# Kernel tuning notes

Measured on AMD Instinct MI355X. Metric: run time of the kernel, lower is better.

## Reference

```python
import jax, jax.numpy as jnp
import numpy as np

N, H, W, PD, HID, NH = 2, 64, 64, 16, 128, 4
EPS = 1e-5


def _bn(x, g, b):
    # training-mode BatchNorm over (N, H, W) with biased variance, channels last
    m = jnp.mean(x, axis=(0, 1, 2), keepdims=True)
    v = jnp.var(x, axis=(0, 1, 2), keepdims=True)
    return (x - m) * jax.lax.rsqrt(v + EPS) * g + b


def _mha(x, in_w, in_b, out_w, out_b, nh):
    # torch nn.MultiheadAttention (batch_first) with packed qkv in_proj
    B, S, E = x.shape
    hd = E // nh
    q, k, v = jnp.split(x @ in_w.T + in_b, 3, axis=-1)
    def heads(t):
        return t.reshape(B, S, nh, hd).transpose(0, 2, 1, 3)  # B,nh,S,hd
    q, k, v = heads(q), heads(k), heads(v)
    a = jax.nn.softmax(jnp.einsum('bnqd,bnkd->bnqk', q, k) / np.float32(np.sqrt(hd)), axis=-1)
    o = jnp.einsum('bnqk,bnkd->bnqd', a, v).transpose(0, 2, 1, 3).reshape(B, S, E)
    return o @ out_w.T + out_b


def setup_inputs():
    key = jax.random.key(0)
    ks = jax.random.split(key, 32)
    def r(i, shape, s=0.1):
        return jax.random.normal(ks[i], shape, dtype=jnp.float32) * s
    mask = (jnp.arange(W) % 2) == 0  # alternating columns kept, M = W//2
    return {
        'kspace': jax.random.normal(ks[0], (N, 2, H, W), dtype=jnp.float32),
        'mask': mask,
        'pre_conv_w': r(1, (PD, 2), 0.5), 'pre_conv_b': r(2, (PD,)),
        'pre_pe_H': r(3, (H, PD)), 'pre_pe_W': r(4, (W, PD)),
        'res_conv1_w': r(5, (PD, PD), 0.2), 'res_conv1_b': r(6, (PD,)),
        'res_bn1_g': 1.0 + r(7, (PD,)), 'res_bn1_b': r(8, (PD,)),
        'res_conv2_w': r(9, (PD, PD), 0.2), 'res_conv2_b': r(10, (PD,)),
        'res_bn2_g': 1.0 + r(11, (PD,)), 'res_bn2_b': r(12, (PD,)),
        'proj_w': r(13, (HID, PD), 0.2), 'proj_b': r(14, (HID,)),
        'enc_in_w': r(15, (3 * HID, HID), 0.08), 'enc_in_b': r(16, (3 * HID,)),
        'enc_out_w': r(17, (HID, HID), 0.08), 'enc_out_b': r(18, (HID,)),
        'dec_pe_H': r(19, (H, HID)), 'dec_pe_W': r(20, (W, HID)),
        'dec_in_w': r(21, (3 * HID, HID), 0.08), 'dec_in_b': r(22, (3 * HID,)),
        'dec_out_w': r(23, (HID, HID), 0.08), 'dec_out_b': r(24, (HID,)),
        'masked_token': r(25, (HID,), 1.0),
        'post_w': r(26, (2, HID), 0.1), 'post_b': r(27, (2,)),
    }


def reference(kspace, mask, pre_conv_w, pre_conv_b, pre_pe_H, pre_pe_W,
              res_conv1_w, res_conv1_b, res_bn1_g, res_bn1_b,
              res_conv2_w, res_conv2_b, res_bn2_g, res_bn2_b,
              proj_w, proj_b, enc_in_w, enc_in_b, enc_out_w, enc_out_b,
              dec_pe_H, dec_pe_W, dec_in_w, dec_in_b, dec_out_w, dec_out_b,
              masked_token, post_w, post_b):
    cols = np.nonzero(np.asarray(mask))[0]  # static sampled columns
    M = cols.shape[0]
    # gather valid columns; channels last: [N, H, M, 2]
    x = kspace.transpose(0, 2, 3, 1)[:, :, cols, :]
    h = x @ pre_conv_w.T + pre_conv_b  # 1x1 conv -> [N, H, M, PD]
    h = h + (pre_pe_H[:, None, :] + pre_pe_W[cols][None, :, :])
    # PixelwiseConstantChannelResNet (1 layer)
    r1 = jax.nn.relu(_bn(h @ res_conv1_w.T + res_conv1_b, res_bn1_g, res_bn1_b))
    r2 = jax.nn.relu(_bn(r1 @ res_conv2_w.T + res_conv2_b, res_bn2_g, res_bn2_b))
    h = jax.nn.relu(h + r2)
    h = h @ proj_w.T + proj_b  # [N, H, M, HID]
    enc = _mha(h.reshape(N, H * M, HID), enc_in_w, enc_in_b, enc_out_w, enc_out_b, NH)
    # scatter: fill unmasked positions with masked_token, masked with encoder output
    dec = jnp.broadcast_to(masked_token, (N, H, W, HID))
    dec = dec.at[:, :, cols, :].set(enc.reshape(N, H, M, HID))
    dec = dec + (dec_pe_H[:, None, :] + dec_pe_W[None, :, :])
    dec = _mha(dec.reshape(N, H * W, HID), dec_in_w, dec_in_b, dec_out_w, dec_out_b, NH)
    out = dec.reshape(N, H, W, HID) @ post_w.T + post_b  # [N, H, W, 2]
    return out.transpose(0, 3, 1, 2)  # [N, 2, H, W]
```

## Files before the change

kernel.cpp:

```cpp
#include <hip/hip_runtime.h>
#include <math.h>

#define N_ 2
#define H_ 64
#define W_ 64
#define M_ 32
#define PD_ 16
#define HID_ 128
#define NH_ 4
#define HD_ 32
#define S_ENC 2048
#define S_DEC 4096
#define EPS_ 1e-5f
#define SCALE_ 0.17677669529663687f
#define SCALE2_ (0.17677669529663687f * 1.4426950408889634f)

#define OFF_H     0
#define OFF_T1    65536
#define OFF_T2    131072
#define OFF_STAT  196608
#define OFF_WP    196672
#define OFF_BP    202816
#define OFF_QBF   203264
#define OFF_KBF   727552
#define OFF_VTBF  1251840
#define OFF_ATTBF 1776128
#define OFF_XBF2  2300416
#define OFF_WBF   2824704

#define WOFF_ENC_OUT 0
#define WOFF_DEC_IN  16384
#define WOFF_DEC_OUT 65536

#define IB_MF   2048
#define IB_WC   320
#define IB_WP   24
#define IB_BP   2
#define IB_TOT  (IB_MF + IB_WC + IB_WP + IB_BP + 1)

typedef short bf16x8 __attribute__((ext_vector_type(8)));
typedef short bf16x4 __attribute__((ext_vector_type(4)));
typedef float f32x4 __attribute__((ext_vector_type(4)));

__device__ __forceinline__ short f2bf(float f) {
  union { float f; unsigned u; } v; v.f = f;
  unsigned r = v.u + 0x7FFFu + ((v.u >> 16) & 1u);
  return (short)(r >> 16);
}

__global__ void k_init(const float* __restrict__ eow, const float* __restrict__ dw,
                       const float* __restrict__ dow, const float* __restrict__ mt,
                       const float* __restrict__ peH, const float* __restrict__ peW,
                       const float* __restrict__ ew, const float* __restrict__ pw,
                       const float* __restrict__ pb, const float* __restrict__ eib,
                       short* __restrict__ wbf, short* __restrict__ xdec,
                       float* __restrict__ wp, float* __restrict__ bp,
                       float* __restrict__ stat) {
  int blk = blockIdx.x, tid = threadIdx.x;
  if (blk < IB_MF) {
    int idx = blk * 256 + tid;
    int j = idx & 127;
    int widx = (idx >> 7) & 31;
    int hh = (idx >> 12) & 63;
    int b = idx >> 18;
    int w = 2 * widx + 1;
    xdec[((size_t)(b * 4096 + hh * 64 + w)) * 128 + j] =
        f2bf(mt[j] + peH[hh * 128 + j] + peW[w * 128 + j]);
  } else if (blk < IB_MF + IB_WC) {
    int idx = (blk - IB_MF) * 256 + tid;
    float v;
    if (idx < 16384) v = eow[idx];
    else if (idx < 65536) v = dw[idx - 16384];
    else v = dow[idx - 65536];
    wbf[idx] = f2bf(v);
  } else if (blk < IB_MF + IB_WC + IB_WP) {
    int e = (blk - IB_MF - IB_WC) * 256 + tid;
    int row = e >> 4, k = e & 15;
    float a = 0.f;
    for (int j = 0; j < 128; j++) a = fmaf(ew[row * 128 + j], pw[j * 16 + k], a);
    wp[e] = a;
  } else if (blk < IB_MF + IB_WC + IB_WP + IB_BP) {
    int row = (blk - IB_MF - IB_WC - IB_WP) * 256 + tid;
    if (row < 384) {
      float a = eib[row];
      for (int j = 0; j < 128; j++) a = fmaf(ew[row * 128 + j], pb[j], a);
      bp[row] = a;
    }
  } else {
    if (tid < 64) stat[tid] = 0.f;
  }
}

__global__ void k_prelin_stats(const float* __restrict__ ks, const float* __restrict__ pcw,
                               const float* __restrict__ pcb, const float* __restrict__ peH,
                               const float* __restrict__ peW, const float* __restrict__ w1,
                               const float* __restrict__ b1, float* __restrict__ h,
                               float* __restrict__ t1, float* __restrict__ stat) {
  int tid = threadIdx.x;
  int pos = blockIdx.x * 256 + tid;
  int m = pos & 31, hh = (pos >> 5) & 63, b = pos >> 11;
  int w = 2 * m;
  float x0 = ks[((b * 2 + 0) * H_ + hh) * W_ + w];
  float x1 = ks[((b * 2 + 1) * H_ + hh) * W_ + w];
  float hv[16], tv[16];
#pragma unroll
  for (int c = 0; c < 16; c++)
    hv[c] = x0 * pcw[c * 2] + x1 * pcw[c * 2 + 1] + pcb[c]
            + peH[hh * PD_ + c] + peW[w * PD_ + c];
#pragma unroll
  for (int c = 0; c < 16; c += 4)
    *(float4*)&h[pos * 16 + c] = make_float4(hv[c], hv[c + 1], hv[c + 2], hv[c + 3]);
#pragma unroll
  for (int c = 0; c < 16; c++) {
    float a = b1[c];
#pragma unroll
    for (int k = 0; k < 16; k++) a = fmaf(hv[k], w1[c * 16 + k], a);
    tv[c] = a;
    t1[pos * 16 + c] = a;
  }
  __shared__ float tl[256][17];
#pragma unroll
  for (int c = 0; c < 16; c++) tl[tid][c] = tv[c];
  __syncthreads();
  int c = tid & 15, g = tid >> 4;
  float s = 0.f, s2 = 0.f;
#pragma unroll
  for (int r = 0; r < 16; r++) {
    float v = tl[g * 16 + r][c];
    s += v; s2 += v * v;
  }
  __shared__ float ps[16][16], ps2[16][16];
  ps[g][c] = s; ps2[g][c] = s2;
  __syncthreads();
  if (tid < 16) {
    float S = 0.f, S2 = 0.f;
#pragma unroll
    for (int g2 = 0; g2 < 16; g2++) { S += ps[g2][tid]; S2 += ps2[g2][tid]; }
    atomicAdd(&stat[tid], S);
    atomicAdd(&stat[16 + tid], S2);
  }
}

__global__ void k_bnlin_stats(const float* __restrict__ t1, const float* __restrict__ stat,
                              const float* __restrict__ g1, const float* __restrict__ bb1,
                              const float* __restrict__ w2, const float* __restrict__ b2,
                              float* __restrict__ t2, float* __restrict__ statw) {
  int tid = threadIdx.x;
  int pos = blockIdx.x * 256 + tid;
  const float inv = 1.f / 4096.f;
  float r[16];
#pragma unroll
  for (int k = 0; k < 16; k++) {
    float mu = stat[k] * inv;
    float var = stat[16 + k] * inv - mu * mu;
    float v = (t1[pos * 16 + k] - mu) * rsqrtf(var + EPS_) * g1[k] + bb1[k];
    r[k] = fmaxf(v, 0.f);
  }
  float tv[16];
#pragma unroll
  for (int c = 0; c < 16; c++) {
    float a = b2[c];
#pragma unroll
    for (int k = 0; k < 16; k++) a = fmaf(r[k], w2[c * 16 + k], a);
    tv[c] = a;
    t2[pos * 16 + c] = a;
  }
  __shared__ float tl[256][17];
#pragma unroll
  for (int c = 0; c < 16; c++) tl[tid][c] = tv[c];
  __syncthreads();
  int c = tid & 15, g = tid >> 4;
  float s = 0.f, s2 = 0.f;
#pragma unroll
  for (int rr = 0; rr < 16; rr++) {
    float v = tl[g * 16 + rr][c];
    s += v; s2 += v * v;
  }
  __shared__ float ps[16][16], ps2[16][16];
  ps[g][c] = s; ps2[g][c] = s2;
  __syncthreads();
  if (tid < 16) {
    float S = 0.f, S2 = 0.f;
#pragma unroll
    for (int g2 = 0; g2 < 16; g2++) { S += ps[g2][tid]; S2 += ps2[g2][tid]; }
    atomicAdd(&statw[32 + tid], S);
    atomicAdd(&statw[48 + tid], S2);
  }
}

__global__ __launch_bounds__(256)
void k_fqkv_enc(const float* __restrict__ h, const float* __restrict__ t2,
                const float* __restrict__ stat, const float* __restrict__ g2,
                const float* __restrict__ bb2, const float* __restrict__ wp,
                const float* __restrict__ bp, short* __restrict__ qbf,
                short* __restrict__ kbf, short* __restrict__ vtbf) {
  int tid = threadIdx.x;
  int p0 = blockIdx.x * 32;
  __shared__ float hf[32][20];
  const float inv = 1.f / 4096.f;
#pragma unroll
  for (int i = 0; i < 2; i++) {
    int idx = tid * 2 + i;
    int lp = idx >> 4, c = idx & 15;
    int pos = p0 + lp;
    float mu = stat[32 + c] * inv;
    float var = stat[48 + c] * inv - mu * mu;
    float v = (t2[pos * 16 + c] - mu) * rsqrtf(var + EPS_) * g2[c] + bb2[c];
    v = fmaxf(v, 0.f);
    hf[lp][c] = fmaxf(h[pos * 16 + c] + v, 0.f);
  }
  __syncthreads();
  int bb = p0 >> 11;
  int sbase = p0 & 2047;
  {
    int col = tid;
    float wc[16];
#pragma unroll
    for (int k = 0; k < 16; k += 4) *(float4*)&wc[k] = *(const float4*)&wp[col * 16 + k];
    float bpv = bp[col];
    int isQ = (col < 128);
    int c2 = isQ ? col : (col - 128);
    int hd = c2 >> 5, d = c2 & 31;
    short* dst = isQ ? qbf : kbf;
    float sc = isQ ? SCALE2_ : 1.f;
    size_t rowb = ((size_t)(bb * 4 + hd) * S_ENC + sbase) * 32 + d;
    for (int lp = 0; lp < 32; lp++) {
      float a = bpv;
#pragma unroll
      for (int k = 0; k < 16; k++) a = fmaf(hf[lp][k], wc[k], a);
      dst[rowb + (size_t)lp * 32] = f2bf(a * sc);
    }
  }
  if (tid < 128) {
    int col = 256 + tid;
    float wc[16];
#pragma unroll
    for (int k = 0; k < 16; k += 4) *(float4*)&wc[k] = *(const float4*)&wp[col * 16 + k];
    float bpv = bp[col];
    int c2 = tid;
    int hd = c2 >> 5, d = c2 & 31;
    size_t rowb = ((size_t)(bb * 4 + hd) * 32 + d) * S_ENC + sbase;
    for (int lp4 = 0; lp4 < 32; lp4 += 4) {
      bf16x4 pk;
#pragma unroll
      for (int r = 0; r < 4; r++) {
        float a = bpv;
#pragma unroll
        for (int k = 0; k < 16; k++) a = fmaf(hf[lp4 + r][k], wc[k], a);
        pk[r] = f2bf(a);
      }
      *(bf16x4*)&vtbf[rowb + lp4] = pk;
    }
  }
}

#define MGEMM_STAGE_AND_FRAGS                                                   \
  __shared__ short As[64 * 128];                                                \
  __shared__ short Wl[64 * 128];                                                \
  int tid = threadIdx.x;                                                        \
  _Pragma("unroll")                                                             \
  for (int i = 0; i < 4; i++) {                                                 \
    int idx = i * 256 + tid;                                                    \
    int row = idx >> 4, c = idx & 15, slot = c ^ (row & 7);                     \
    *(bf16x8*)&As[row * 128 + slot * 8] =                                       \
        *(const bf16x8*)&abf[(size_t)(rb + row) * 128 + c * 8];                 \
    *(bf16x8*)&Wl[row * 128 + slot * 8] =                                       \
        *(const bf16x8*)&wbf[(size_t)(ob + row) * 128 + c * 8];                 \
  }                                                                             \
  __syncthreads();                                                              \
  int lane = tid & 63, wv = tid >> 6;                                           \
  int l15 = lane & 15, quad = lane >> 4;                                        \
  int m0 = wv * 16;                                                             \
  f32x4 acc[4];                                                                 \
  acc[0] = acc[1] = acc[2] = acc[3] = (f32x4){0.f, 0.f, 0.f, 0.f};              \
  _Pragma("unroll")                                                             \
  for (int kk = 0; kk < 4; kk++) {                                              \
    int sl = ((kk * 4 + quad) ^ (l15 & 7)) * 8;                                 \
    bf16x8 af = *(const bf16x8*)&As[(m0 + l15) * 128 + sl];                     \
    _Pragma("unroll")                                                           \
    for (int nt = 0; nt < 4; nt++) {                                            \
      bf16x8 wf = *(const bf16x8*)&Wl[(nt * 16 + l15) * 128 + sl];              \
      acc[nt] = __builtin_amdgcn_mfma_f32_16x16x32_bf16(af, wf, acc[nt], 0, 0, 0); \
    }                                                                           \
  }

__global__ __launch_bounds__(256)
void k_mgemm_qkv_dec(const short* __restrict__ abf, const short* __restrict__ wbf,
                     const float* __restrict__ bias, short* __restrict__ qbf,
                     short* __restrict__ kbf, short* __restrict__ vtbf) {
  const int S = 4096;
  int rb = blockIdx.x * 64, ob = blockIdx.y * 64;
  MGEMM_STAGE_AND_FRAGS
#pragma unroll
  for (int nt = 0; nt < 4; nt++) {
    int col = ob + nt * 16 + l15;
    float bv = bias[col];
    if (ob < 128) {
      int hd = col >> 5, d = col & 31;
#pragma unroll
      for (int r = 0; r < 4; r++) {
        int grow = rb + m0 + quad * 4 + r;
        int bb = grow >> 12, s = grow & (S - 1);
        qbf[((size_t)(bb * 4 + hd) * S + s) * 32 + d] =
            f2bf((acc[nt][r] + bv) * SCALE2_);
      }
    } else if (ob < 256) {
      int c2 = col - 128, hd = c2 >> 5, d = c2 & 31;
#pragma unroll
      for (int r = 0; r < 4; r++) {
        int grow = rb + m0 + quad * 4 + r;
        int bb = grow >> 12, s = grow & (S - 1);
        kbf[((size_t)(bb * 4 + hd) * S + s) * 32 + d] = f2bf(acc[nt][r] + bv);
      }
    } else {
      int c2 = col - 256, hd = c2 >> 5, d = c2 & 31;
      int grow0 = rb + m0 + quad * 4;
      int bb = grow0 >> 12, s0 = grow0 & (S - 1);
      bf16x4 pk;
#pragma unroll
      for (int r = 0; r < 4; r++) pk[r] = f2bf(acc[nt][r] + bv);
      *(bf16x4*)&vtbf[((size_t)(bb * 4 + hd) * 32 + d) * S + s0] = pk;
    }
  }
}

__global__ __launch_bounds__(256)
void k_mgemm_out_enc(const short* __restrict__ abf, const short* __restrict__ wbf,
                     const float* __restrict__ bias, const float* __restrict__ peH,
                     const float* __restrict__ peW, short* __restrict__ xdec) {
  int rb = blockIdx.x * 64, ob = blockIdx.y * 64;
  MGEMM_STAGE_AND_FRAGS
#pragma unroll
  for (int nt = 0; nt < 4; nt++) {
    int col = ob + nt * 16 + l15;
    float bv = bias[col];
#pragma unroll
    for (int r = 0; r < 4; r++) {
      int grow = rb + m0 + quad * 4 + r;
      int bb = grow >> 11, rem = grow & 2047;
      int hhh = rem >> 5, m = rem & 31, w = 2 * m;
      xdec[((size_t)(bb * 4096 + hhh * 64 + w)) * 128 + col] =
          f2bf(acc[nt][r] + bv + peH[hhh * 128 + col] + peW[w * 128 + col]);
    }
  }
}

__global__ __launch_bounds__(256)
void k_mgemm_out_post(const short* __restrict__ abf, const short* __restrict__ wbf,
                      const float* __restrict__ bias, const float* __restrict__ pw,
                      const float* __restrict__ pb, float* __restrict__ outp) {
  int rb = blockIdx.x * 64;
  __shared__ short As[64 * 128];
  __shared__ short Wl[128 * 128];
  int tid = threadIdx.x;
#pragma unroll
  for (int i = 0; i < 4; i++) {
    int idx = i * 256 + tid;
    int row = idx >> 4, c = idx & 15, slot = c ^ (row & 7);
    *(bf16x8*)&As[row * 128 + slot * 8] =
        *(const bf16x8*)&abf[(size_t)(rb + row) * 128 + c * 8];
  }
#pragma unroll
  for (int i = 0; i < 8; i++) {
    int idx = i * 256 + tid;
    int row = idx >> 4, c = idx & 15, slot = c ^ (row & 7);
    *(bf16x8*)&Wl[row * 128 + slot * 8] =
        *(const bf16x8*)&wbf[(size_t)row * 128 + c * 8];
  }
  __syncthreads();
  int lane = tid & 63, wv = tid >> 6;
  int l15 = lane & 15, quad = lane >> 4;
  int m0 = wv * 16;
  f32x4 acc[8];
#pragma unroll
  for (int nt = 0; nt < 8; nt++) acc[nt] = (f32x4){0.f, 0.f, 0.f, 0.f};
#pragma unroll
  for (int kk = 0; kk < 4; kk++) {
    int sl = ((kk * 4 + quad) ^ (l15 & 7)) * 8;
    bf16x8 af = *(const bf16x8*)&As[(m0 + l15) * 128 + sl];
#pragma unroll
    for (int nt = 0; nt < 8; nt++) {
      bf16x8 wf = *(const bf16x8*)&Wl[(nt * 16 + l15) * 128 + sl];
      acc[nt] = __builtin_amdgcn_mfma_f32_16x16x32_bf16(af, wf, acc[nt], 0, 0, 0);
    }
  }
  float bv[8], pw0[8], pw1[8];
#pragma unroll
  for (int nt = 0; nt < 8; nt++) {
    int col = nt * 16 + l15;
    bv[nt] = bias[col];
    pw0[nt] = pw[col];
    pw1[nt] = pw[128 + col];
  }
  float pb0 = pb[0], pb1 = pb[1];
#pragma unroll
  for (int r = 0; r < 4; r++) {
    float pc0 = 0.f, pc1 = 0.f;
#pragma unroll
    for (int nt = 0; nt < 8; nt++) {
      float yv = acc[nt][r] + bv[nt];
      pc0 = fmaf(yv, pw0[nt], pc0);
      pc1 = fmaf(yv, pw1[nt], pc1);
    }
    pc0 += __shfl_xor(pc0, 1); pc0 += __shfl_xor(pc0, 2);
    pc0 += __shfl_xor(pc0, 4); pc0 += __shfl_xor(pc0, 8);
    pc1 += __shfl_xor(pc1, 1); pc1 += __shfl_xor(pc1, 2);
    pc1 += __shfl_xor(pc1, 4); pc1 += __shfl_xor(pc1, 8);
    if (l15 == 0) {
      int grow = rb + m0 + quad * 4 + r;
      int bb = grow >> 12, hw = grow & 4095;
      outp[(size_t)(bb * 2 + 0) * 4096 + hw] = pc0 + pb0;
      outp[(size_t)(bb * 2 + 1) * 4096 + hw] = pc1 + pb1;
    }
  }
}

template <int S>
__global__ __launch_bounds__(1024)
__attribute__((amdgpu_waves_per_eu(8)))
void k_attn11(const short* __restrict__ qbf, const short* __restrict__ kbf,
              const short* __restrict__ vtbf, short* __restrict__ outb) {
  __shared__ __align__(16) char smem[65536];
  short* kb4 = (short*)smem;
  short* vt4 = (short*)(smem + 32768);
  float* abuf = (float*)smem;
  float* lb   = (float*)(smem + 24576);

  int qt = blockIdx.x, hh = blockIdx.y, b = blockIdx.z;
  int tid = threadIdx.x;
  int lane = tid & 63;
  int wv = tid >> 6;
  int qtr = wv >> 2;
  int wv4 = wv & 3;
  int l15 = lane & 15, quad = lane >> 4;
  int t256 = tid & 255;

  int bh = b * NH_ + hh;
  const short* kg = kbf + (size_t)bh * S * 32;
  const short* vg = vtbf + (size_t)bh * 32 * S;
  short* kbh = kb4 + qtr * 2048;
  short* vth = vt4 + qtr * 2048;

  bf16x8 qf = *(const bf16x8*)&qbf[((size_t)bh * S + qt * 64 + wv4 * 16 + l15) * 32
                                   + quad * 8];

  f32x4 acc[2];
  acc[0] = (f32x4){0.f, 0.f, 0.f, 0.f};
  acc[1] = (f32x4){0.f, 0.f, 0.f, 0.f};
  float lpart = 0.f;

  int srowK = t256 >> 2, schK = t256 & 3;
  int slotK = schK ^ ((srowK >> 1) & 3);
  int srowV = t256 >> 3, sslV = t256 & 7;
  int sgV = sslV ^ (srowV & 7);
  int gbV = ((sgV >> 2) << 5) + ((sgV & 3) << 2);

  int kq0 = qtr * (S / 4);
  int kxor = (l15 >> 1) & 3;
  int vsl = l15 & 7;

  const short* kgp = kg + (size_t)(kq0 + srowK) * 32 + schK * 8;
  const short* vgp0 = vg + (size_t)srowV * S + kq0 + gbV;
  const short* vgp1 = vgp0 + 16;
  short* kdst = kbh + srowK * 32 + slotK * 8;
  short* vdst = vth + srowV * 64 + sslV * 8;

  bf16x8 krg = *(const bf16x8*)kgp;
  bf16x4 vr0 = *(const bf16x4*)vgp0;
  bf16x4 vr1 = *(const bf16x4*)vgp1;

  constexpr int NIT = S / 256;
  for (int it = 0; it < NIT; ++it) {
    int co = (it & 1) << 13;
    *(bf16x8*)(kdst + co) = krg;
    *(bf16x8*)(vdst + co) = __builtin_shufflevector(vr0, vr1, 0, 1, 2, 3, 4, 5, 6, 7);
    if (it + 1 < NIT) {
      kgp += 64 * 32;
      vgp0 += 64;
      vgp1 += 64;
      krg = *(const bf16x8*)kgp;
      vr0 = *(const bf16x4*)vgp0;
      vr1 = *(const bf16x4*)vgp1;
    }
    asm volatile("s_waitcnt lgkmcnt(0)" ::: "memory");
    __builtin_amdgcn_s_barrier();
    asm volatile("" ::: "memory");

    const short* kbhc = kbh + co;
    const short* vthc = vth + co;

    f32x4 s[4];
#pragma unroll
    for (int t = 0; t < 4; t++) {
      bf16x8 kf = *(const bf16x8*)&kbhc[(t * 16 + l15) * 32 + ((quad ^ kxor) * 8)];
      s[t] = __builtin_amdgcn_mfma_f32_16x16x32_bf16(
          kf, qf, (f32x4){0.f, 0.f, 0.f, 0.f}, 0, 0, 0);
    }

    float pe[4][4];
#pragma unroll
    for (int t = 0; t < 4; t++) {
      pe[t][0] = __builtin_exp2f(s[t][0]);
      pe[t][1] = __builtin_exp2f(s[t][1]);
      pe[t][2] = __builtin_exp2f(s[t][2]);
      pe[t][3] = __builtin_exp2f(s[t][3]);
      lpart += (pe[t][0] + pe[t][1]) + (pe[t][2] + pe[t][3]);
    }

#pragma unroll
    for (int kh = 0; kh < 2; kh++) {
      union { unsigned u[4]; bf16x8 v; } pf;
      asm("v_cvt_pk_bf16_f32 %0, %1, %2"
          : "=v"(pf.u[0]) : "v"(pe[2 * kh][0]), "v"(pe[2 * kh][1]));
      asm("v_cvt_pk_bf16_f32 %0, %1, %2"
          : "=v"(pf.u[1]) : "v"(pe[2 * kh][2]), "v"(pe[2 * kh][3]));
      asm("v_cvt_pk_bf16_f32 %0, %1, %2"
          : "=v"(pf.u[2]) : "v"(pe[2 * kh + 1][0]), "v"(pe[2 * kh + 1][1]));
      asm("v_cvt_pk_bf16_f32 %0, %1, %2"
          : "=v"(pf.u[3]) : "v"(pe[2 * kh + 1][2]), "v"(pe[2 * kh + 1][3]));
#pragma unroll
      for (int nt = 0; nt < 2; nt++) {
        bf16x8 vf = *(const bf16x8*)&vthc[(nt * 16 + l15) * 64
                                          + (((kh * 4 + quad) ^ vsl) * 8)];
        acc[nt] = __builtin_amdgcn_mfma_f32_16x16x32_bf16(vf, pf.v, acc[nt], 0, 0, 0);
      }
    }
  }

  lpart += __shfl_xor(lpart, 16);
  lpart += __shfl_xor(lpart, 32);

  __syncthreads();
  if (qtr > 0) {
#pragma unroll
    for (int nt = 0; nt < 2; nt++)
#pragma unroll
      for (int r = 0; r < 4; r++)
        abuf[(qtr - 1) * 2048 + wv4 * 512 + (nt * 16 + quad * 4 + r) * 16 + l15] =
            acc[nt][r];
    if (quad == 0) lb[(qtr - 1) * 64 + wv4 * 16 + l15] = lpart;
  }
  __syncthreads();
  if (qtr == 0) {
    int li = wv4 * 16 + l15;
    float ltot = lpart + lb[li] + lb[64 + li] + lb[128 + li];
    float inv = 1.f / ltot;
    int base = wv4 * 512;
    short* op = outb + ((size_t)(b * S + qt * 64 + wv4 * 16 + l15)) * 128 + hh * 32;
#pragma unroll
    for (int nt = 0; nt < 2; nt++) {
      bf16x4 pk;
#pragma unroll
      for (int r = 0; r < 4; r++) {
        int d = nt * 16 + quad * 4 + r;
        float v = acc[nt][r] + abuf[base + d * 16 + l15]
                + abuf[2048 + base + d * 16 + l15]
                + abuf[4096 + base + d * 16 + l15];
        pk[r] = f2bf(v * inv);
      }
      *(bf16x4*)&op[nt * 16 + quad * 4] = pk;
    }
  }
}

extern "C" void kernel_launch(void* const* d_in, const int* in_sizes, int n_in,
                              void* d_out, int out_size, void* d_ws, size_t ws_size,
                              hipStream_t stream) {
  const float* ks        = (const float*)d_in[0];
  const float* pre_conv_w = (const float*)d_in[2];
  const float* pre_conv_b = (const float*)d_in[3];
  const float* pre_pe_H   = (const float*)d_in[4];
  const float* pre_pe_W   = (const float*)d_in[5];
  const float* w1  = (const float*)d_in[6];
  const float* b1  = (const float*)d_in[7];
  const float* g1  = (const float*)d_in[8];
  const float* bb1 = (const float*)d_in[9];
  const float* w2  = (const float*)d_in[10];
  const float* b2  = (const float*)d_in[11];
  const float* g2  = (const float*)d_in[12];
  const float* bb2 = (const float*)d_in[13];
  const float* proj_w = (const float*)d_in[14];
  const float* proj_b = (const float*)d_in[15];
  const float* enc_in_w  = (const float*)d_in[16];
  const float* enc_in_b  = (const float*)d_in[17];
  const float* enc_out_w = (const float*)d_in[18];
  const float* enc_out_b = (const float*)d_in[19];
  const float* dec_pe_H  = (const float*)d_in[20];
  const float* dec_pe_W  = (const float*)d_in[21];
  const float* dec_in_w  = (const float*)d_in[22];
  const float* dec_in_b  = (const float*)d_in[23];
  const float* dec_out_w = (const float*)d_in[24];
  const float* dec_out_b = (const float*)d_in[25];
  const float* masked_token = (const float*)d_in[26];
  const float* post_w = (const float*)d_in[27];
  const float* post_b = (const float*)d_in[28];
  float* out = (float*)d_out;

  float* ws    = (float*)d_ws;
  float* h     = ws + OFF_H;
  float* t1    = ws + OFF_T1;
  float* t2    = ws + OFF_T2;
  float* stat  = ws + OFF_STAT;
  float* wp    = ws + OFF_WP;
  float* bp    = ws + OFF_BP;
  short* qbf   = (short*)(ws + OFF_QBF);
  short* kbfb  = (short*)(ws + OFF_KBF);
  short* vtbfb = (short*)(ws + OFF_VTBF);
  short* attbf = (short*)(ws + OFF_ATTBF);
  short* xbf2  = (short*)(ws + OFF_XBF2);
  short* wbf   = (short*)(ws + OFF_WBF);

  k_init<<<IB_TOT, 256, 0, stream>>>(enc_out_w, dec_in_w, dec_out_w, masked_token,
                                     dec_pe_H, dec_pe_W, enc_in_w, proj_w, proj_b,
                                     enc_in_b, wbf, xbf2, wp, bp, stat);
  k_prelin_stats<<<16, 256, 0, stream>>>(ks, pre_conv_w, pre_conv_b, pre_pe_H,
                                         pre_pe_W, w1, b1, h, t1, stat);
  k_bnlin_stats<<<16, 256, 0, stream>>>(t1, stat, g1, bb1, w2, b2, t2, stat);
  k_fqkv_enc<<<128, 256, 0, stream>>>(h, t2, stat, g2, bb2, wp, bp,
                                      qbf, kbfb, vtbfb);
  k_attn11<S_ENC><<<dim3(S_ENC / 64, NH_, N_), 1024, 0, stream>>>(qbf, kbfb, vtbfb, attbf);
  k_mgemm_out_enc<<<dim3(S_ENC * N_ / 64, 2), 256, 0, stream>>>(
      attbf, wbf + WOFF_ENC_OUT, enc_out_b, dec_pe_H, dec_pe_W, xbf2);
  k_mgemm_qkv_dec<<<dim3(S_DEC * N_ / 64, 6), 256, 0, stream>>>(
      xbf2, wbf + WOFF_DEC_IN, dec_in_b, qbf, kbfb, vtbfb);
  k_attn11<S_DEC><<<dim3(S_DEC / 64, NH_, N_), 1024, 0, stream>>>(qbf, kbfb, vtbfb, attbf);
  k_mgemm_out_post<<<S_DEC * N_ / 64, 256, 0, stream>>>(
      attbf, wbf + WOFF_DEC_OUT, dec_out_b, post_w, post_b, out);
}
```

Before: 203.7 us.

## Store V in MFMA-fragment order and read K/V straight from global in attention

The V projection writers now emit V^T in a tiled layout that matches the MFMA B-operand fragment order. This lets the attention kernel load K and V fragments directly from global/L2 with contiguous 16-byte loads, dropping the LDS staging, double-buffering and per-iteration barriers. LDS use shrinks to the final reduction buffer and the waves-per-EU hint is lowered to 4. The trade-off is that every wave now reloads K/V from cache with no LDS sharing across the four waves of a quarter, which adds global load traffic and latency exposure.

```diff
diff --git a/kernel.cpp b/kernel.cpp
--- a/kernel.cpp
+++ b/kernel.cpp
@@ -239,8 +239,14 @@
     float bpv = bp[col];
     int c2 = tid;
     int hd = c2 >> 5, d = c2 & 31;
-    size_t rowb = ((size_t)(bb * 4 + hd) * 32 + d) * S_ENC + sbase;
+    int nt2 = d >> 4, l15b = d & 15;
+    int bh = bb * 4 + hd;
+    int tile = sbase >> 6, kh = (sbase >> 5) & 1;
+    size_t base = ((((size_t)bh * (S_ENC / 64) + tile) * 2 + kh) * 2 + nt2) * 512
+                  + l15b * 8;
     for (int lp4 = 0; lp4 < 32; lp4 += 4) {
+      int s0 = sbase + lp4;
+      int e_hi = (s0 >> 4) & 1, q4 = (s0 >> 2) & 3;
       bf16x4 pk;
 #pragma unroll
       for (int r = 0; r < 4; r++) {
@@ -249,7 +255,7 @@
         for (int k = 0; k < 16; k++) a = fmaf(hf[lp4 + r][k], wc[k], a);
         pk[r] = f2bf(a);
       }
-      *(bf16x4*)&vtbf[rowb + lp4] = pk;
+      *(bf16x4*)&vtbf[base + q4 * 128 + e_hi * 4] = pk;
     }
   }
 }
@@ -314,12 +320,16 @@
       }
     } else {
       int c2 = col - 256, hd = c2 >> 5, d = c2 & 31;
+      int nt2 = d >> 4, l15b = d & 15;
       int grow0 = rb + m0 + quad * 4;
       int bb = grow0 >> 12, s0 = grow0 & (S - 1);
+      int tile = s0 >> 6, kh = (s0 >> 5) & 1;
+      int e_hi = (s0 >> 4) & 1, q4 = (s0 >> 2) & 3;
       bf16x4 pk;
 #pragma unroll
       for (int r = 0; r < 4; r++) pk[r] = f2bf(acc[nt][r] + bv);
-      *(bf16x4*)&vtbf[((size_t)(bb * 4 + hd) * 32 + d) * S + s0] = pk;
+      *(bf16x4*)&vtbf[((((size_t)(bb * 4 + hd) * (S / 64) + tile) * 2 + kh) * 2 + nt2)
+                          * 512 + q4 * 128 + l15b * 8 + e_hi * 4] = pk;
     }
   }
 }
@@ -417,12 +427,10 @@
 
 template <int S>
 __global__ __launch_bounds__(1024)
-__attribute__((amdgpu_waves_per_eu(8)))
-void k_attn11(const short* __restrict__ qbf, const short* __restrict__ kbf,
+__attribute__((amdgpu_waves_per_eu(4)))
+void k_attn14(const short* __restrict__ qbf, const short* __restrict__ kbf,
               const short* __restrict__ vtbf, short* __restrict__ outb) {
-  __shared__ __align__(16) char smem[65536];
-  short* kb4 = (short*)smem;
-  short* vt4 = (short*)(smem + 32768);
+  __shared__ __align__(16) char smem[25344];
   float* abuf = (float*)smem;
   float* lb   = (float*)(smem + 24576);
 
@@ -433,13 +441,12 @@
   int qtr = wv >> 2;
   int wv4 = wv & 3;
   int l15 = lane & 15, quad = lane >> 4;
-  int t256 = tid & 255;
 
   int bh = b * NH_ + hh;
-  const short* kg = kbf + (size_t)bh * S * 32;
-  const short* vg = vtbf + (size_t)bh * 32 * S;
-  short* kbh = kb4 + qtr * 2048;
-  short* vth = vt4 + qtr * 2048;
+  const short* kgp = kbf + (size_t)bh * S * 32 + (size_t)qtr * (S / 4) * 32
+                     + (l15 * 32 + quad * 8);
+  const short* vgp = vtbf + (size_t)bh * S * 32 + (size_t)qtr * (S / 4) * 32
+                     + (quad * 128 + l15 * 8);
 
   bf16x8 qf = *(const bf16x8*)&qbf[((size_t)bh * S + qt * 64 + wv4 * 16 + l15) * 32
                                    + quad * 8];
@@ -449,53 +456,25 @@
   acc[1] = (f32x4){0.f, 0.f, 0.f, 0.f};
   float lpart = 0.f;
 
-  int srowK = t256 >> 2, schK = t256 & 3;
-  int slotK = schK ^ ((srowK >> 1) & 3);
-  int srowV = t256 >> 3, sslV = t256 & 7;
-  int sgV = sslV ^ (srowV & 7);
-  int gbV = ((sgV >> 2) << 5) + ((sgV & 3) << 2);
-
-  int kq0 = qtr * (S / 4);
-  int kxor = (l15 >> 1) & 3;
-  int vsl = l15 & 7;
-
-  const short* kgp = kg + (size_t)(kq0 + srowK) * 32 + schK * 8;
-  const short* vgp0 = vg + (size_t)srowV * S + kq0 + gbV;
-  const short* vgp1 = vgp0 + 16;
-  short* kdst = kbh + srowK * 32 + slotK * 8;
-  short* vdst = vth + srowV * 64 + sslV * 8;
-
-  bf16x8 krg = *(const bf16x8*)kgp;
-  bf16x4 vr0 = *(const bf16x4*)vgp0;
-  bf16x4 vr1 = *(const bf16x4*)vgp1;
-
   constexpr int NIT = S / 256;
+#pragma unroll 2
   for (int it = 0; it < NIT; ++it) {
-    int co = (it & 1) << 13;
-    *(bf16x8*)(kdst + co) = krg;
-    *(bf16x8*)(vdst + co) = __builtin_shufflevector(vr0, vr1, 0, 1, 2, 3, 4, 5, 6, 7);
-    if (it + 1 < NIT) {
-      kgp += 64 * 32;
-      vgp0 += 64;
-      vgp1 += 64;
-      krg = *(const bf16x8*)kgp;
-      vr0 = *(const bf16x4*)vgp0;
-      vr1 = *(const bf16x4*)vgp1;
-    }
-    asm volatile("s_waitcnt lgkmcnt(0)" ::: "memory");
-    __builtin_amdgcn_s_barrier();
-    asm volatile("" ::: "memory");
-
-    const short* kbhc = kbh + co;
-    const short* vthc = vth + co;
+    bf16x8 kf0 = *(const bf16x8*)(kgp);
+    bf16x8 kf1 = *(const bf16x8*)(kgp + 512);
+    bf16x8 kf2 = *(const bf16x8*)(kgp + 1024);
+    bf16x8 kf3 = *(const bf16x8*)(kgp + 1536);
+    bf16x8 vf00 = *(const bf16x8*)(vgp);
+    bf16x8 vf01 = *(const bf16x8*)(vgp + 512);
+    bf16x8 vf10 = *(const bf16x8*)(vgp + 1024);
+    bf16x8 vf11 = *(const bf16x8*)(vgp + 1536);
+    kgp += 2048;
+    vgp += 2048;
 
     f32x4 s[4];
-#pragma unroll
-    for (int t = 0; t < 4; t++) {
-      bf16x8 kf = *(const bf16x8*)&kbhc[(t * 16 + l15) * 32 + ((quad ^ kxor) * 8)];
-      s[t] = __builtin_amdgcn_mfma_f32_16x16x32_bf16(
-          kf, qf, (f32x4){0.f, 0.f, 0.f, 0.f}, 0, 0, 0);
-    }
+    s[0] = __builtin_amdgcn_mfma_f32_16x16x32_bf16(kf0, qf, (f32x4){0.f,0.f,0.f,0.f}, 0, 0, 0);
+    s[1] = __builtin_amdgcn_mfma_f32_16x16x32_bf16(kf1, qf, (f32x4){0.f,0.f,0.f,0.f}, 0, 0, 0);
+    s[2] = __builtin_amdgcn_mfma_f32_16x16x32_bf16(kf2, qf, (f32x4){0.f,0.f,0.f,0.f}, 0, 0, 0);
+    s[3] = __builtin_amdgcn_mfma_f32_16x16x32_bf16(kf3, qf, (f32x4){0.f,0.f,0.f,0.f}, 0, 0, 0);
 
     float pe[4][4];
 #pragma unroll
@@ -507,23 +486,23 @@
       lpart += (pe[t][0] + pe[t][1]) + (pe[t][2] + pe[t][3]);
     }
 
-#pragma unroll
-    for (int kh = 0; kh < 2; kh++) {
+    {
       union { unsigned u[4]; bf16x8 v; } pf;
-      asm("v_cvt_pk_bf16_f32 %0, %1, %2"
-          : "=v"(pf.u[0]) : "v"(pe[2 * kh][0]), "v"(pe[2 * kh][1]));
-      asm("v_cvt_pk_bf16_f32 %0, %1, %2"
-          : "=v"(pf.u[1]) : "v"(pe[2 * kh][2]), "v"(pe[2 * kh][3]));
-      asm("v_cvt_pk_bf16_f32 %0, %1, %2"
-          : "=v"(pf.u[2]) : "v"(pe[2 * kh + 1][0]), "v"(pe[2 * kh + 1][1]));
-      asm("v_cvt_pk_bf16_f32 %0, %1, %2"
-          : "=v"(pf.u[3]) : "v"(pe[2 * kh + 1][2]), "v"(pe[2 * kh + 1][3]));
-#pragma unroll
-      for (int nt = 0; nt < 2; nt++) {
-        bf16x8 vf = *(const bf16x8*)&vthc[(nt * 16 + l15) * 64
-                                          + (((kh * 4 + quad) ^ vsl) * 8)];
-        acc[nt] = __builtin_amdgcn_mfma_f32_16x16x32_bf16(vf, pf.v, acc[nt], 0, 0, 0);
-      }
+      asm("v_cvt_pk_bf16_f32 %0, %1, %2" : "=v"(pf.u[0]) : "v"(pe[0][0]), "v"(pe[0][1]));
+      asm("v_cvt_pk_bf16_f32 %0, %1, %2" : "=v"(pf.u[1]) : "v"(pe[0][2]), "v"(pe[0][3]));
+      asm("v_cvt_pk_bf16_f32 %0, %1, %2" : "=v"(pf.u[2]) : "v"(pe[1][0]), "v"(pe[1][1]));
+      asm("v_cvt_pk_bf16_f32 %0, %1, %2" : "=v"(pf.u[3]) : "v"(pe[1][2]), "v"(pe[1][3]));
+      acc[0] = __builtin_amdgcn_mfma_f32_16x16x32_bf16(vf00, pf.v, acc[0], 0, 0, 0);
+      acc[1] = __builtin_amdgcn_mfma_f32_16x16x32_bf16(vf01, pf.v, acc[1], 0, 0, 0);
+    }
+    {
+      union { unsigned u[4]; bf16x8 v; } pf;
+      asm("v_cvt_pk_bf16_f32 %0, %1, %2" : "=v"(pf.u[0]) : "v"(pe[2][0]), "v"(pe[2][1]));
+      asm("v_cvt_pk_bf16_f32 %0, %1, %2" : "=v"(pf.u[1]) : "v"(pe[2][2]), "v"(pe[2][3]));
+      asm("v_cvt_pk_bf16_f32 %0, %1, %2" : "=v"(pf.u[2]) : "v"(pe[3][0]), "v"(pe[3][1]));
+      asm("v_cvt_pk_bf16_f32 %0, %1, %2" : "=v"(pf.u[3]) : "v"(pe[3][2]), "v"(pe[3][3]));
+      acc[0] = __builtin_amdgcn_mfma_f32_16x16x32_bf16(vf10, pf.v, acc[0], 0, 0, 0);
+      acc[1] = __builtin_amdgcn_mfma_f32_16x16x32_bf16(vf11, pf.v, acc[1], 0, 0, 0);
     }
   }
 
@@ -618,12 +597,12 @@
   k_bnlin_stats<<<16, 256, 0, stream>>>(t1, stat, g1, bb1, w2, b2, t2, stat);
   k_fqkv_enc<<<128, 256, 0, stream>>>(h, t2, stat, g2, bb2, wp, bp,
                                       qbf, kbfb, vtbfb);
-  k_attn11<S_ENC><<<dim3(S_ENC / 64, NH_, N_), 1024, 0, stream>>>(qbf, kbfb, vtbfb, attbf);
+  k_attn14<S_ENC><<<dim3(S_ENC / 64, NH_, N_), 1024, 0, stream>>>(qbf, kbfb, vtbfb, attbf);
   k_mgemm_out_enc<<<dim3(S_ENC * N_ / 64, 2), 256, 0, stream>>>(
       attbf, wbf + WOFF_ENC_OUT, enc_out_b, dec_pe_H, dec_pe_W, xbf2);
   k_mgemm_qkv_dec<<<dim3(S_DEC * N_ / 64, 6), 256, 0, stream>>>(
       xbf2, wbf + WOFF_DEC_IN, dec_in_b, qbf, kbfb, vtbfb);
-  k_attn11<S_DEC><<<dim3(S_DEC / 64, NH_, N_), 1024, 0, stream>>>(qbf, kbfb, vtbfb, attbf);
+  k_attn14<S_DEC><<<dim3(S_DEC / 64, NH_, N_), 1024, 0, stream>>>(qbf, kbfb, vtbfb, attbf);
   k_mgemm_out_post<<<S_DEC * N_ / 64, 256, 0, stream>>>(
       attbf, wbf + WOFF_DEC_OUT, dec_out_b, post_w, post_b, out);
 }
```

Result: slower. 219.8 us (+7.9%).
